# Optimization experiments

Hardware: AMD Instinct MI355X
Metric: run time of the kernel (lower is better)

## Reference

```python
import jax, jax.numpy as jnp
import numpy as np

N = 262144   # nodes
E = 1048576  # edges (avg degree 4)
DIN = 64     # input node features
H = 128      # hidden channels
DE = 32      # edge feature dim
EPS = 1e-5


def setup_inputs() -> dict:
    key = jax.random.key(0)
    ks = jax.random.split(key, 12)
    s = 0.05
    return {
        "x": jax.random.normal(ks[0], (N, DIN), jnp.float32),
        "edge_attr": jax.random.normal(ks[1], (E, DE), jnp.float32),
        "W_enter": jax.random.normal(ks[2], (H, DIN), jnp.float32) * s,
        "b_enter": jnp.zeros((H,), jnp.float32),
        "W1": jax.random.normal(ks[3], (H, H + DE), jnp.float32) * s,
        "att_l": jax.random.normal(ks[4], (H,), jnp.float32) * s,
        "att_r": jax.random.normal(ks[5], (H,), jnp.float32) * s,
        "W2": jax.random.normal(ks[6], (H, H), jnp.float32) * s,
        "b_conv": jnp.zeros((H,), jnp.float32),
        "W_ih": jax.random.normal(ks[7], (3 * H, H), jnp.float32) * s,
        "W_hh": jax.random.normal(ks[8], (3 * H, H), jnp.float32) * s,
        "b_ih": jnp.zeros((3 * H,), jnp.float32),
        "b_hh": jnp.zeros((3 * H,), jnp.float32),
        "edge_index": jax.random.randint(ks[9], (2, E), 0, N, jnp.int32),
    }


def _segment_softmax(logits, seg, num_segments):
    m = jax.ops.segment_max(logits, seg, num_segments=num_segments)
    e = jnp.exp(logits - m[seg])
    d = jax.ops.segment_sum(e, seg, num_segments=num_segments)
    return e / d[seg]


def reference(x, edge_attr, W_enter, b_enter, W1, att_l, att_r, W2, b_conv,
              W_ih, W_hh, b_ih, b_hh, edge_index):
    n = x.shape[0]
    src, dst = edge_index[0], edge_index[1]  # x_j = x[src], aggregate to dst

    # lin_enter + leaky_relu
    x = jax.nn.leaky_relu(x @ W_enter.T + b_enter)

    # Edge2dConv message: leaky_relu(lin1([x_j, edge_attr]))
    m = jax.nn.leaky_relu(jnp.concatenate([x[src], edge_attr], axis=-1) @ W1.T)  # [E,H]
    alpha = jax.nn.leaky_relu(m @ att_l + x[dst] @ att_r)  # [E]
    alpha = _segment_softmax(alpha, dst, n)
    msg = (m @ W2.T) * alpha[:, None]
    out = jax.ops.segment_sum(msg, dst, num_segments=n) + b_conv

    # elu, then GRUCell(h_in=out_elu, hidden=x)
    h = jax.nn.elu(out)
    gi = h @ W_ih.T + b_ih
    gh = x @ W_hh.T + b_hh
    ir, iz, inn = jnp.split(gi, 3, axis=-1)
    hr, hz, hn = jnp.split(gh, 3, axis=-1)
    r = jax.nn.sigmoid(ir + hr)
    z = jax.nn.sigmoid(iz + hz)
    ncand = jnp.tanh(inn + r * hn)
    x = jax.nn.relu((1.0 - z) * ncand + z * x)

    # layer_norm (no affine)
    mu = jnp.mean(x, axis=-1, keepdims=True)
    var = jnp.mean(jnp.square(x - mu), axis=-1, keepdims=True)
    return (x - mu) / jnp.sqrt(var + EPS)
```

## Files before the change

### kernel.cpp

```cpp
#include <hip/hip_runtime.h>
#include <stdint.h>

#define HD  128
#define DIN 64
#define DE  32

typedef unsigned int u32; typedef unsigned short u16; typedef unsigned char u8;
typedef short s16x8 __attribute__((ext_vector_type(8)));
typedef float f32x4 __attribute__((ext_vector_type(4)));
typedef float f32x2 __attribute__((ext_vector_type(2)));

#define MFMA16(a,b,c) __builtin_amdgcn_mfma_f32_16x16x32_bf16((a),(b),(c),0,0,0)

__device__ __forceinline__ float lrelu(float x){ return x > 0.f ? x : 0.01f*x; }
__device__ __forceinline__ float sigmoidf_(float x){ return 1.f/(1.f + __expf(-x)); }
__device__ __forceinline__ float tanhf_(float x){
    float t = fminf(fmaxf(x, -15.f), 15.f);
    float e = __expf(2.f*t);
    return (e - 1.f)/(e + 1.f);
}
__device__ __forceinline__ float eluf_(float x){ return x > 0.f ? x : expm1f(x); }

__device__ __forceinline__ u16 f32_to_bf16(float x){
    u32 u = __float_as_uint(x);
    u += 0x7FFFu + ((u >> 16) & 1u);
    return (u16)(u >> 16);
}
__device__ __forceinline__ float bf16lo(u32 u){ return __uint_as_float((u & 0xFFFFu) << 16); }
__device__ __forceinline__ float bf16hi(u32 u){ return __uint_as_float(u & 0xFFFF0000u); }
__device__ __forceinline__ float bf16f(u16 h){ return __uint_as_float(((u32)h) << 16); }
__device__ __forceinline__ u32 pk2(float a, float b){
    return (u32)f32_to_bf16(a) | ((u32)f32_to_bf16(b) << 16);
}
__device__ __forceinline__ u8 hw_f8(float v){
    return (u8)__builtin_amdgcn_cvt_pk_fp8_f32(v, v, 0, false);
}
__device__ __forceinline__ f32x2 hw_f8_dec2(u32 u){
    return __builtin_amdgcn_cvt_pk_f32_fp8((int)u, false);
}
__device__ __forceinline__ f32x2 hw_f8_dec2_hi(u32 u){
    return __builtin_amdgcn_cvt_pk_f32_fp8((int)u, true);
}

__device__ __forceinline__ float wave_max(float v){
    #pragma unroll
    for (int o = 32; o > 0; o >>= 1) v = fmaxf(v, __shfl_xor(v, o, 64));
    return v;
}
__device__ __forceinline__ float wave_sum(float v){
    #pragma unroll
    for (int o = 32; o > 0; o >>= 1) v += __shfl_xor(v, o, 64);
    return v;
}
__device__ __forceinline__ float dot8_bf16(uint4 v, const float* __restrict__ al){
    float d = 0.f;
    d = fmaf(bf16lo(v.x), al[0], d); d = fmaf(bf16hi(v.x), al[1], d);
    d = fmaf(bf16lo(v.y), al[2], d); d = fmaf(bf16hi(v.y), al[3], d);
    d = fmaf(bf16lo(v.z), al[4], d); d = fmaf(bf16hi(v.z), al[5], d);
    d = fmaf(bf16lo(v.w), al[6], d); d = fmaf(bf16hi(v.w), al[7], d);
    return d;
}

__global__ void k_prep(const float* __restrict__ W1, const float* __restrict__ W2,
                       const float* __restrict__ Went,
                       const float* __restrict__ Wih, const float* __restrict__ Whh,
                       u16* __restrict__ W1b, u16* __restrict__ W2b,
                       u16* __restrict__ Wentb, u16* __restrict__ Bg)
{
    int i = blockIdx.x*256 + threadIdx.x;
    if (i < 20480){ W1b[i] = f32_to_bf16(W1[i]); return; }
    i -= 20480;
    if (i < 16384){ W2b[i] = f32_to_bf16(W2[i]); return; }
    i -= 16384;
    if (i < 8192){ Wentb[i] = f32_to_bf16(Went[i]); return; }
    i -= 8192;
    if (i < 131072){
        int col = i >> 8, k = i & 255;
        int g = col >> 7, j = col & 127;
        float v;
        if      (g == 0) v = (k < 128) ? Wih[j*128 + k]        : Whh[j*128 + k - 128];
        else if (g == 1) v = (k < 128) ? Wih[(128+j)*128 + k]  : Whh[(128+j)*128 + k - 128];
        else if (g == 2) v = (k < 128) ? Wih[(256+j)*128 + k]  : 0.f;
        else             v = (k < 128) ? 0.f                   : Whh[(256+j)*128 + k - 128];
        Bg[i] = f32_to_bf16(v);
    }
}

__global__ void k_zero2(int* __restrict__ a, int* __restrict__ b, int n){
    int i = blockIdx.x*256 + threadIdx.x;
    if (i < n){ a[i] = 0; b[i] = 0; }
}

__global__ __launch_bounds__(256, 2) void k_enter_mfma(
    const float* __restrict__ x, const u16* __restrict__ Wb, const float* __restrict__ be,
    const float* __restrict__ att_r, u16* __restrict__ Ag, float* __restrict__ r_out, int N)
{
    __shared__ __align__(16) u8 sA[64*144];
    __shared__ __align__(16) u8 sO[64*272];
    int t = threadIdx.x, w = t >> 6, lane = t & 63, l15 = lane & 15, l4 = lane >> 4;
    int tile = blockIdx.x;

    s16x8 bfr[2][2];
    #pragma unroll
    for (int kf = 0; kf < 2; ++kf)
        #pragma unroll
        for (int cf = 0; cf < 2; ++cf)
            bfr[kf][cf] = *(const s16x8*)(Wb + (size_t)(w*32 + cf*16 + l15)*64 + kf*32 + l4*8);

    int el = t >> 2, q = t & 3;
    size_t n = (size_t)tile*64 + el;
    {
        const float4* xs = (const float4*)(x + n*64 + q*16);
        float4 f0 = xs[0], f1 = xs[1], f2 = xs[2], f3 = xs[3];
        uint4 o0, o1;
        o0.x = pk2(f0.x,f0.y); o0.y = pk2(f0.z,f0.w); o0.z = pk2(f1.x,f1.y); o0.w = pk2(f1.z,f1.w);
        o1.x = pk2(f2.x,f2.y); o1.y = pk2(f2.z,f2.w); o1.z = pk2(f3.x,f3.y); o1.w = pk2(f3.z,f3.w);
        *(uint4*)(sA + el*144 + q*32)      = o0;
        *(uint4*)(sA + el*144 + q*32 + 16) = o1;
    }
    __syncthreads();

    f32x4 acc[4][2];
    #pragma unroll
    for (int rf = 0; rf < 4; ++rf){ acc[rf][0] = (f32x4)0.f; acc[rf][1] = (f32x4)0.f; }
    #pragma unroll
    for (int kf = 0; kf < 2; ++kf){
        s16x8 a[4];
        #pragma unroll
        for (int rf = 0; rf < 4; ++rf)
            a[rf] = *(const s16x8*)(sA + (rf*16 + l15)*144 + kf*64 + l4*16);
        #pragma unroll
        for (int rf = 0; rf < 4; ++rf){
            acc[rf][0] = MFMA16(a[rf], bfr[kf][0], acc[rf][0]);
            acc[rf][1] = MFMA16(a[rf], bfr[kf][1], acc[rf][1]);
        }
    }
    float b0 = be[w*32 + l15], b1 = be[w*32 + 16 + l15];
    #pragma unroll
    for (int rf = 0; rf < 4; ++rf)
        #pragma unroll
        for (int r = 0; r < 4; ++r){
            int row = rf*16 + l4*4 + r;
            *(u16*)(sO + row*272 + (w*32 + l15)*2)      = f32_to_bf16(lrelu(acc[rf][0][r] + b0));
            *(u16*)(sO + row*272 + (w*32 + 16 + l15)*2) = f32_to_bf16(lrelu(acc[rf][1][r] + b1));
        }
    __syncthreads();

    float dot = 0.f;
    #pragma unroll
    for (int i = 0; i < 4; ++i){
        uint4 v = *(const uint4*)(sO + el*272 + q*64 + 16*i);
        ((uint4*)Ag)[n*32 + 16 + q*4 + i] = v;
        dot += dot8_bf16(v, att_r + q*32 + 8*i);
    }
    dot += __shfl_xor(dot, 1); dot += __shfl_xor(dot, 2);
    if (q == 0) r_out[n] = dot;
}

__global__ void k_hist(const int* __restrict__ dst, int* __restrict__ deg, int E){
    int e = blockIdx.x*256 + threadIdx.x;
    if (e < E) atomicAdd(&deg[dst[e]], 1);
}
__global__ __launch_bounds__(256) void k_scan_a(
    const int* __restrict__ deg, int* __restrict__ rs, int* __restrict__ btot, int N)
{
    __shared__ int sd[256];
    int b = blockIdx.x, t = threadIdx.x;
    int base = b*1024 + t*4;
    int d0 = deg[base], d1 = deg[base+1], d2 = deg[base+2], d3 = deg[base+3];
    int s = d0 + d1 + d2 + d3;
    sd[t] = s; __syncthreads();
    for (int o = 1; o < 256; o <<= 1){
        int v = (t >= o) ? sd[t-o] : 0;
        __syncthreads();
        sd[t] += v;
        __syncthreads();
    }
    int ex = sd[t] - s;
    rs[base]   = ex;
    rs[base+1] = ex + d0;
    rs[base+2] = ex + d0 + d1;
    rs[base+3] = ex + d0 + d1 + d2;
    if (t == 0) btot[b] = sd[255];
}
__global__ __launch_bounds__(256) void k_scan_b(const int* __restrict__ btot, int* __restrict__ bbase){
    __shared__ int sd[256];
    int t = threadIdx.x;
    int s = btot[t];
    sd[t] = s; __syncthreads();
    for (int o = 1; o < 256; o <<= 1){
        int v = (t >= o) ? sd[t-o] : 0;
        __syncthreads();
        sd[t] += v;
        __syncthreads();
    }
    bbase[t] = sd[t] - s;
}
__global__ void k_scan_c(int* __restrict__ rs, const int* __restrict__ bbase, int N, int E){
    int i = blockIdx.x*256 + threadIdx.x;
    if (i < N) rs[i] += bbase[i >> 10];
    if (i == 0) rs[N] = E;
}
__global__ void k_scatter(const int* __restrict__ dst, const int* __restrict__ rs,
                          int* __restrict__ cnt, int* __restrict__ epos, int E){
    int e = blockIdx.x*256 + threadIdx.x;
    if (e >= E) return;
    int d = dst[e];
    int pos = rs[d] + atomicAdd(&cnt[d], 1);
    epos[e] = pos;
}

__global__ __launch_bounds__(512, 4) void k_edge_mfma(
    const u16* __restrict__ Ag, const float* __restrict__ ea,
    const u16* __restrict__ W1b, const float* __restrict__ att_l,
    const float* __restrict__ r_dst, const int* __restrict__ src, const int* __restrict__ dst,
    const int* __restrict__ epos,
    u8* __restrict__ m, float* __restrict__ alpha, int ntiles, int E)
{
    __shared__ __align__(16) u8 sA[64*336];
    __shared__ __align__(16) u8 sM[64*144];
    int t = threadIdx.x, w = t >> 6, lane = t & 63, l15 = lane & 15, l4 = lane >> 4;

    s16x8 bfr[5];
    #pragma unroll
    for (int kf = 0; kf < 5; ++kf)
        bfr[kf] = *(const s16x8*)(W1b + (size_t)(w*16 + l15)*160 + kf*32 + l4*8);

    int el = t >> 3, q = t & 7;
    int stride = gridDim.x;
    int tile = blockIdx.x;

    uint4 cx0, cx1;
    u32 ce0, ce1;
    int   pe = 0;
    float rdv = 0.f;
    {
        int e = tile*64 + el;
        if (tile < ntiles && e < E){
            int sn = src[e];
            const uint4* xs = (const uint4*)Ag + (size_t)sn*32 + 16 + q*2;
            cx0 = xs[0]; cx1 = xs[1];
            float4 f = *(const float4*)(ea + (size_t)e*32 + q*4);
            ce0 = pk2(f.x, f.y); ce1 = pk2(f.z, f.w);
            pe  = epos[e];
            rdv = r_dst[dst[e]];
        }
    }

    int   ptile = -1;
    int   pe_prev = 0;
    float rdv_prev = 0.f;

    for (; tile < ntiles; tile += stride){
        int e = tile*64 + el;
        if (e < E){
            uint4* d = (uint4*)(sA + el*336 + q*32);
            d[0] = cx0; d[1] = cx1;
            *(u32*)(sA + el*336 + 256 + q*8)     = ce0;
            *(u32*)(sA + el*336 + 256 + q*8 + 4) = ce1;
        }
        int pe_cur = pe; float rdv_cur = rdv;

        int nt = tile + stride;
        if (nt < ntiles){
            int e2 = nt*64 + el;
            if (e2 < E){
                int sn = src[e2];
                const uint4* xs = (const uint4*)Ag + (size_t)sn*32 + 16 + q*2;
                cx0 = xs[0]; cx1 = xs[1];
                float4 f = *(const float4*)(ea + (size_t)e2*32 + q*4);
                ce0 = pk2(f.x, f.y); ce1 = pk2(f.z, f.w);
                pe  = epos[e2];
                rdv = r_dst[dst[e2]];
            }
        }

        if (ptile >= 0){
            int ep = ptile*64 + el;
            if (ep < E){
                uint4 v = *(const uint4*)(sM + el*144 + q*16);
                ((uint4*)m)[(size_t)pe_prev*8 + q] = v;
                u32 ws[4] = {v.x, v.y, v.z, v.w};
                float dotv = 0.f;
                #pragma unroll
                for (int i = 0; i < 4; ++i){
                    f32x2 fa = hw_f8_dec2(ws[i]);
                    f32x2 fb = hw_f8_dec2_hi(ws[i]);
                    const float* al = att_l + q*16 + i*4;
                    dotv = fmaf(fa.x, al[0], dotv); dotv = fmaf(fa.y, al[1], dotv);
                    dotv = fmaf(fb.x, al[2], dotv); dotv = fmaf(fb.y, al[3], dotv);
                }
                dotv += __shfl_xor(dotv, 1); dotv += __shfl_xor(dotv, 2); dotv += __shfl_xor(dotv, 4);
                if (q == 0) alpha[pe_prev] = lrelu(dotv + rdv_prev);
            }
        }
        __syncthreads();

        f32x4 acc[4];
        #pragma unroll
        for (int rf = 0; rf < 4; ++rf) acc[rf] = (f32x4)0.f;
        #pragma unroll
        for (int kf = 0; kf < 5; ++kf){
            s16x8 a[4];
            #pragma unroll
            for (int rf = 0; rf < 4; ++rf)
                a[rf] = *(const s16x8*)(sA + (rf*16 + l15)*336 + kf*64 + l4*16);
            #pragma unroll
            for (int rf = 0; rf < 4; ++rf)
                acc[rf] = MFMA16(a[rf], bfr[kf], acc[rf]);
        }

        int col = w*16 + l15;
        #pragma unroll
        for (int rf = 0; rf < 4; ++rf)
            #pragma unroll
            for (int r = 0; r < 4; ++r){
                int row = rf*16 + l4*4 + r;
                sM[row*144 + col] = hw_f8(lrelu(acc[rf][r]));
            }
        __syncthreads();

        ptile = tile; pe_prev = pe_cur; rdv_prev = rdv_cur;
    }

    if (ptile >= 0){
        int ep = ptile*64 + el;
        if (ep < E){
            uint4 v = *(const uint4*)(sM + el*144 + q*16);
            ((uint4*)m)[(size_t)pe_prev*8 + q] = v;
            u32 ws[4] = {v.x, v.y, v.z, v.w};
            float dotv = 0.f;
            #pragma unroll
            for (int i = 0; i < 4; ++i){
                f32x2 fa = hw_f8_dec2(ws[i]);
                f32x2 fb = hw_f8_dec2_hi(ws[i]);
                const float* al = att_l + q*16 + i*4;
                dotv = fmaf(fa.x, al[0], dotv); dotv = fmaf(fa.y, al[1], dotv);
                dotv = fmaf(fb.x, al[2], dotv); dotv = fmaf(fb.y, al[3], dotv);
            }
            dotv += __shfl_xor(dotv, 1); dotv += __shfl_xor(dotv, 2); dotv += __shfl_xor(dotv, 4);
            if (q == 0) alpha[pe_prev] = lrelu(dotv + rdv_prev);
        }
    }
}

__global__ __launch_bounds__(256) void k_agg(
    const int* __restrict__ rs,
    const float* __restrict__ alpha, const u8* __restrict__ m,
    u16* __restrict__ a_out, int N)
{
    int wid  = (blockIdx.x*256 + threadIdx.x) >> 6;
    int lane = threadIdx.x & 63;
    if (wid >= N) return;
    int s = rs[wid], t = rs[wid+1];
    int deg = t - s;
    float ax = 0.f, ay = 0.f;
    if (deg > 0 && deg <= 64){
        float av = -1e38f;
        if (lane < deg) av = alpha[s + lane];
        float mx = wave_max(av);
        float ev = (lane < deg) ? __expf(av - mx) : 0.f;
        float ssum = wave_sum(ev);
        float wreg = ev / ssum;
        int k = 0;
        for (; k + 2 <= deg; k += 2){
            float w0 = __shfl(wreg, k);
            float w1 = __shfl(wreg, k + 1);
            u32 u0 = *(const u16*)(m + (size_t)(s + k)*HD + 2*lane);
            u32 u1 = *(const u16*)(m + (size_t)(s + k + 1)*HD + 2*lane);
            f32x2 f0 = hw_f8_dec2(u0);
            f32x2 f1 = hw_f8_dec2(u1);
            ax = fmaf(w0, f0.x, ax); ay = fmaf(w0, f0.y, ay);
            ax = fmaf(w1, f1.x, ax); ay = fmaf(w1, f1.y, ay);
        }
        if (k < deg){
            float w0 = __shfl(wreg, k);
            u32 u0 = *(const u16*)(m + (size_t)(s + k)*HD + 2*lane);
            f32x2 f0 = hw_f8_dec2(u0);
            ax = fmaf(w0, f0.x, ax); ay = fmaf(w0, f0.y, ay);
        }
    } else if (deg > 64){
        float mx = -1e38f;
        for (int k = lane; k < deg; k += 64) mx = fmaxf(mx, alpha[s + k]);
        mx = wave_max(mx);
        float ssum = 0.f;
        for (int k = lane; k < deg; k += 64) ssum += __expf(alpha[s + k] - mx);
        ssum = wave_sum(ssum);
        float inv = 1.f / ssum;
        for (int k = 0; k < deg; ++k){
            float wgt = __expf(alpha[s + k] - mx) * inv;
            u32 u0 = *(const u16*)(m + (size_t)(s + k)*HD + 2*lane);
            f32x2 f0 = hw_f8_dec2(u0);
            ax = fmaf(wgt, f0.x, ax);
            ay = fmaf(wgt, f0.y, ay);
        }
    }
    *(u32*)(a_out + (size_t)wid*HD + 2*lane) = pk2(ax, ay);
}

__global__ __launch_bounds__(256, 2) void k_conv2_mfma(
    const u16* __restrict__ a, const u16* __restrict__ W2b, const float* __restrict__ bc,
    u16* __restrict__ Ag, int N)
{
    __shared__ __align__(16) u8 sA[64*272];
    __shared__ __align__(16) u8 sO[64*272];
    int t = threadIdx.x, w = t >> 6, lane = t & 63, l15 = lane & 15, l4 = lane >> 4;
    int tile = blockIdx.x;

    s16x8 bfr[4][2];
    #pragma unroll
    for (int kf = 0; kf < 4; ++kf)
        #pragma unroll
        for (int cf = 0; cf < 2; ++cf)
            bfr[kf][cf] = *(const s16x8*)(W2b + (size_t)(w*32 + cf*16 + l15)*128 + kf*32 + l4*8);

    int el = t >> 2, q = t & 3;
    size_t n = (size_t)tile*64 + el;
    {
        const uint4* as = (const uint4*)(a + n*HD) + q*4;
        uint4 v0 = as[0], v1 = as[1], v2 = as[2], v3 = as[3];
        uint4* d = (uint4*)(sA + el*272 + q*64);
        d[0] = v0; d[1] = v1; d[2] = v2; d[3] = v3;
    }
    __syncthreads();

    f32x4 acc[4][2];
    #pragma unroll
    for (int rf = 0; rf < 4; ++rf){ acc[rf][0] = (f32x4)0.f; acc[rf][1] = (f32x4)0.f; }
    #pragma unroll
    for (int kf = 0; kf < 4; ++kf){
        s16x8 av[4];
        #pragma unroll
        for (int rf = 0; rf < 4; ++rf)
            av[rf] = *(const s16x8*)(sA + (rf*16 + l15)*272 + kf*64 + l4*16);
        #pragma unroll
        for (int rf = 0; rf < 4; ++rf){
            acc[rf][0] = MFMA16(av[rf], bfr[kf][0], acc[rf][0]);
            acc[rf][1] = MFMA16(av[rf], bfr[kf][1], acc[rf][1]);
        }
    }
    float b0 = bc[w*32 + l15], b1 = bc[w*32 + 16 + l15];
    #pragma unroll
    for (int rf = 0; rf < 4; ++rf)
        #pragma unroll
        for (int r = 0; r < 4; ++r){
            int row = rf*16 + l4*4 + r;
            *(u16*)(sO + row*272 + (w*32 + l15)*2)      = f32_to_bf16(eluf_(acc[rf][0][r] + b0));
            *(u16*)(sO + row*272 + (w*32 + 16 + l15)*2) = f32_to_bf16(eluf_(acc[rf][1][r] + b1));
        }
    __syncthreads();
    #pragma unroll
    for (int i = 0; i < 4; ++i){
        uint4 v = *(const uint4*)(sO + el*272 + q*64 + 16*i);
        ((uint4*)Ag)[n*32 + q*4 + i] = v;
    }
}

__global__ __launch_bounds__(512, 3) void k_gru_mfma(
    const u16* __restrict__ Ag, const u16* __restrict__ Bg,
    const float* __restrict__ bih, const float* __restrict__ bhh,
    float* __restrict__ out, int N, int ntiles)
{
    __shared__ __align__(16) u8 sA[32*528];
    __shared__ __align__(16) float sOut[32*132];
    int t = threadIdx.x, w = t >> 6, lane = t & 63, l15 = lane & 15, l4 = lane >> 4;

    s16x8 bfr0[8], bfr1[8], bfr2[4], bfr3[4];
    {
        int jc = w*16 + l15;
        #pragma unroll
        for (int kf = 0; kf < 8; ++kf){
            bfr0[kf] = *(const s16x8*)(Bg + (size_t)(jc)*256       + kf*32 + l4*8);
            bfr1[kf] = *(const s16x8*)(Bg + (size_t)(128 + jc)*256 + kf*32 + l4*8);
        }
        #pragma unroll
        for (int kf = 0; kf < 4; ++kf){
            bfr2[kf] = *(const s16x8*)(Bg + (size_t)(256 + jc)*256 + kf*32 + l4*8);
            bfr3[kf] = *(const s16x8*)(Bg + (size_t)(384 + jc)*256 + (kf+4)*32 + l4*8);
        }
    }
    int j = w*16 + l15;
    float rb = bih[j] + bhh[j];
    float zb = bih[128 + j] + bhh[128 + j];
    float ib = bih[256 + j];
    float hb = bhh[256 + j];

    int el = t >> 4, part = t & 15;
    int stride = gridDim.x;
    int tile = blockIdx.x;
    uint4 pv0, pv1;
    if (tile < ntiles){
        const uint4* gsrc = (const uint4*)Ag + ((size_t)tile*32 + el)*32 + part*2;
        pv0 = gsrc[0]; pv1 = gsrc[1];
    }

    for (; tile < ntiles; tile += stride){
        {
            uint4* d = (uint4*)(sA + el*528 + part*32);
            d[0] = pv0; d[1] = pv1;
        }
        __syncthreads();

        int nt = tile + stride;
        if (nt < ntiles){
            const uint4* gsrc = (const uint4*)Ag + ((size_t)nt*32 + el)*32 + part*2;
            pv0 = gsrc[0]; pv1 = gsrc[1];
        }

        f32x4 acc[2][4];
        #pragma unroll
        for (int rf = 0; rf < 2; ++rf)
            #pragma unroll
            for (int g = 0; g < 4; ++g) acc[rf][g] = (f32x4)0.f;
        #pragma unroll
        for (int kf = 0; kf < 8; ++kf){
            s16x8 a0 = *(const s16x8*)(sA + l15*528 + kf*64 + l4*16);
            s16x8 a1 = *(const s16x8*)(sA + (16 + l15)*528 + kf*64 + l4*16);
            acc[0][0] = MFMA16(a0, bfr0[kf], acc[0][0]);
            acc[1][0] = MFMA16(a1, bfr0[kf], acc[1][0]);
            acc[0][1] = MFMA16(a0, bfr1[kf], acc[0][1]);
            acc[1][1] = MFMA16(a1, bfr1[kf], acc[1][1]);
            if (kf < 4){
                acc[0][2] = MFMA16(a0, bfr2[kf], acc[0][2]);
                acc[1][2] = MFMA16(a1, bfr2[kf], acc[1][2]);
            } else {
                acc[0][3] = MFMA16(a0, bfr3[kf-4], acc[0][3]);
                acc[1][3] = MFMA16(a1, bfr3[kf-4], acc[1][3]);
            }
        }
        #pragma unroll
        for (int rf = 0; rf < 2; ++rf)
            #pragma unroll
            for (int r = 0; r < 4; ++r){
                int rl = rf*16 + l4*4 + r;
                float rr = sigmoidf_(acc[rf][0][r] + rb);
                float zz = sigmoidf_(acc[rf][1][r] + zb);
                float iv = acc[rf][2][r] + ib;
                float hv = acc[rf][3][r] + hb;
                float nc = tanhf_(iv + rr*hv);
                float xej = bf16f(*(const u16*)(sA + rl*528 + 256 + 2*j));
                float v = (1.f - zz)*nc + zz*xej;
                v = fmaxf(v, 0.f);
                sOut[rl*132 + j] = v;
            }
        __syncthreads();
        {
            int row = t >> 4, sub = t & 15;
            const float* rp = sOut + row*132 + sub*8;
            float v0 = rp[0], v1 = rp[1], v2 = rp[2], v3 = rp[3];
            float v4 = rp[4], v5 = rp[5], v6 = rp[6], v7 = rp[7];
            float s1 = v0+v1+v2+v3+v4+v5+v6+v7;
            float s2 = v0*v0+v1*v1+v2*v2+v3*v3+v4*v4+v5*v5+v6*v6+v7*v7;
            #pragma unroll
            for (int o = 1; o < 16; o <<= 1){ s1 += __shfl_xor(s1, o); s2 += __shfl_xor(s2, o); }
            float mu  = s1 * (1.f/128.f);
            float var = s2 * (1.f/128.f) - mu*mu;
            var = fmaxf(var, 0.f);
            float rsd = rsqrtf(var + 1e-5f);
            float* op = out + ((size_t)tile*32 + row)*128 + sub*8;
            float4 o0, o1;
            o0.x = (v0-mu)*rsd; o0.y = (v1-mu)*rsd; o0.z = (v2-mu)*rsd; o0.w = (v3-mu)*rsd;
            o1.x = (v4-mu)*rsd; o1.y = (v5-mu)*rsd; o1.z = (v6-mu)*rsd; o1.w = (v7-mu)*rsd;
            ((float4*)op)[0] = o0; ((float4*)op)[1] = o1;
        }
        __syncthreads();
    }
}

extern "C" void kernel_launch(void* const* d_in, const int* in_sizes, int n_in,
                              void* d_out, int out_size, void* d_ws, size_t ws_size,
                              hipStream_t stream)
{
    const float* x       = (const float*)d_in[0];
    const float* ea      = (const float*)d_in[1];
    const float* W_enter = (const float*)d_in[2];
    const float* b_enter = (const float*)d_in[3];
    const float* W1      = (const float*)d_in[4];
    const float* att_l   = (const float*)d_in[5];
    const float* att_r   = (const float*)d_in[6];
    const float* W2      = (const float*)d_in[7];
    const float* b_conv  = (const float*)d_in[8];
    const float* W_ih    = (const float*)d_in[9];
    const float* W_hh    = (const float*)d_in[10];
    const float* b_ih    = (const float*)d_in[11];
    const float* b_hh    = (const float*)d_in[12];
    const int*   eidx    = (const int*)d_in[13];

    int N = in_sizes[0] / DIN;
    int E = in_sizes[13] / 2;
    const int* src = eidx;
    const int* dst = eidx + E;
    float* out = (float*)d_out;

    size_t off = 0;
    char* base = (char*)d_ws;
    auto alloc = [&](size_t bytes) -> char* {
        char* p = base + off;
        off = (off + bytes + 255) & ~(size_t)255;
        return p;
    };
    u16*   Ag    = (u16*)  alloc((size_t)N*256*2);
    float* r_dst = (float*)alloc((size_t)N*4);
    float* alpha = (float*)alloc((size_t)E*4);
    int*   deg   = (int*)  alloc((size_t)N*4);
    int*   rs    = (int*)  alloc((size_t)(N+1)*4);
    int*   cnt   = (int*)  alloc((size_t)N*4);
    int*   epos  = (int*)  alloc((size_t)E*4);
    int*   btot  = (int*)  alloc(1024);
    int*   bbase = (int*)  alloc(1024);
    u16*   W1b   = (u16*)  alloc(20480*2);
    u16*   W2b   = (u16*)  alloc(16384*2);
    u16*   Wentb = (u16*)  alloc(8192*2);
    u16*   Bg    = (u16*)  alloc(131072*2);
    u8*    mbuf  = (u8*)   alloc((size_t)E*HD);

    u16* a_agg = (u16*)out;

    int ntiles_n64 = N/64, ntiles_e = (E + 63)/64, ntiles_g = N/32;

    k_prep   <<<(176128+255)/256, 256, 0, stream>>>(W1, W2, W_enter, W_ih, W_hh, W1b, W2b, Wentb, Bg);
    k_zero2  <<<(N+255)/256, 256, 0, stream>>>(deg, cnt, N);
    k_enter_mfma<<<ntiles_n64, 256, 0, stream>>>(x, Wentb, b_enter, att_r, Ag, r_dst, N);
    k_hist   <<<(E+255)/256, 256, 0, stream>>>(dst, deg, E);
    k_scan_a <<<N/1024, 256, 0, stream>>>(deg, rs, btot, N);
    k_scan_b <<<1, 256, 0, stream>>>(btot, bbase);
    k_scan_c <<<(N+255)/256, 256, 0, stream>>>(rs, bbase, N, E);
    k_scatter<<<(E+255)/256, 256, 0, stream>>>(dst, rs, cnt, epos, E);
    k_edge_mfma<<<1024, 512, 0, stream>>>(Ag, ea, W1b, att_l, r_dst, src, dst, epos,
                                          mbuf, alpha, ntiles_e, E);
    k_agg    <<<(N+3)/4, 256, 0, stream>>>(rs, alpha, mbuf, a_agg, N);
    k_conv2_mfma<<<ntiles_n64, 256, 0, stream>>>(a_agg, W2b, b_conv, Ag, N);
    k_gru_mfma  <<<2048, 512, 0, stream>>>(Ag, Bg, b_ih, b_hh, out, N, ntiles_g);
}
```

Measured before the change: 597.2 us.

## Run GRU GEMM in fp8 and split node buffer into bf16 features and fp8 GRU input

```diff
diff --git a/kernel.cpp b/kernel.cpp
--- a/kernel.cpp
+++ b/kernel.cpp
@@ -6,11 +6,13 @@
 #define DE  32
 
 typedef unsigned int u32; typedef unsigned short u16; typedef unsigned char u8;
+typedef long i64_;
 typedef short s16x8 __attribute__((ext_vector_type(8)));
 typedef float f32x4 __attribute__((ext_vector_type(4)));
 typedef float f32x2 __attribute__((ext_vector_type(2)));
 
-#define MFMA16(a,b,c) __builtin_amdgcn_mfma_f32_16x16x32_bf16((a),(b),(c),0,0,0)
+#define MFMA16(a,b,c)  __builtin_amdgcn_mfma_f32_16x16x32_bf16((a),(b),(c),0,0,0)
+#define MFMAF8(a,b,c)  __builtin_amdgcn_mfma_f32_16x16x32_fp8_fp8((a),(b),(c),0,0,0)
 
 __device__ __forceinline__ float lrelu(float x){ return x > 0.f ? x : 0.01f*x; }
 __device__ __forceinline__ float sigmoidf_(float x){ return 1.f/(1.f + __expf(-x)); }
@@ -34,6 +36,11 @@
 }
 __device__ __forceinline__ u8 hw_f8(float v){
     return (u8)__builtin_amdgcn_cvt_pk_fp8_f32(v, v, 0, false);
+}
+__device__ __forceinline__ u32 hw_f8x4(float a, float b, float c, float d){
+    u32 r = (u32)__builtin_amdgcn_cvt_pk_fp8_f32(a, b, 0, false);
+    r = (u32)__builtin_amdgcn_cvt_pk_fp8_f32(c, d, (int)r, true);
+    return r;
 }
 __device__ __forceinline__ f32x2 hw_f8_dec2(u32 u){
     return __builtin_amdgcn_cvt_pk_f32_fp8((int)u, false);
@@ -65,7 +72,7 @@
                        const float* __restrict__ Went,
                        const float* __restrict__ Wih, const float* __restrict__ Whh,
                        u16* __restrict__ W1b, u16* __restrict__ W2b,
-                       u16* __restrict__ Wentb, u16* __restrict__ Bg)
+                       u16* __restrict__ Wentb, u8* __restrict__ Bgf8)
 {
     int i = blockIdx.x*256 + threadIdx.x;
     if (i < 20480){ W1b[i] = f32_to_bf16(W1[i]); return; }
@@ -82,7 +89,7 @@
         else if (g == 1) v = (k < 128) ? Wih[(128+j)*128 + k]  : Whh[(128+j)*128 + k - 128];
         else if (g == 2) v = (k < 128) ? Wih[(256+j)*128 + k]  : 0.f;
         else             v = (k < 128) ? 0.f                   : Whh[(256+j)*128 + k - 128];
-        Bg[i] = f32_to_bf16(v);
+        Bgf8[i] = hw_f8(v);
     }
 }
 
@@ -93,7 +100,8 @@
 
 __global__ __launch_bounds__(256, 2) void k_enter_mfma(
     const float* __restrict__ x, const u16* __restrict__ Wb, const float* __restrict__ be,
-    const float* __restrict__ att_r, u16* __restrict__ Ag, float* __restrict__ r_out, int N)
+    const float* __restrict__ att_r, u16* __restrict__ xeb, u8* __restrict__ Agru,
+    float* __restrict__ r_out, int N)
 {
     __shared__ __align__(16) u8 sA[64*144];
     __shared__ __align__(16) u8 sO[64*272];
@@ -150,8 +158,16 @@
     #pragma unroll
     for (int i = 0; i < 4; ++i){
         uint4 v = *(const uint4*)(sO + el*272 + q*64 + 16*i);
-        ((uint4*)Ag)[n*32 + 16 + q*4 + i] = v;
-        dot += dot8_bf16(v, att_r + q*32 + 8*i);
+        ((uint4*)xeb)[n*16 + q*4 + i] = v;
+        float f0 = bf16lo(v.x), f1 = bf16hi(v.x), f2 = bf16lo(v.y), f3 = bf16hi(v.y);
+        float f4 = bf16lo(v.z), f5 = bf16hi(v.z), f6 = bf16lo(v.w), f7 = bf16hi(v.w);
+        const float* al = att_r + q*32 + 8*i;
+        dot = fmaf(f0, al[0], dot); dot = fmaf(f1, al[1], dot);
+        dot = fmaf(f2, al[2], dot); dot = fmaf(f3, al[3], dot);
+        dot = fmaf(f4, al[4], dot); dot = fmaf(f5, al[5], dot);
+        dot = fmaf(f6, al[6], dot); dot = fmaf(f7, al[7], dot);
+        uint2 p; p.x = hw_f8x4(f0, f1, f2, f3); p.y = hw_f8x4(f4, f5, f6, f7);
+        *(uint2*)(Agru + n*256 + 128 + q*32 + i*8) = p;
     }
     dot += __shfl_xor(dot, 1); dot += __shfl_xor(dot, 2);
     if (q == 0) r_out[n] = dot;
@@ -211,7 +227,7 @@
 }
 
 __global__ __launch_bounds__(512, 4) void k_edge_mfma(
-    const u16* __restrict__ Ag, const float* __restrict__ ea,
+    const u16* __restrict__ xeb, const float* __restrict__ ea,
     const u16* __restrict__ W1b, const float* __restrict__ att_l,
     const float* __restrict__ r_dst, const int* __restrict__ src, const int* __restrict__ dst,
     const int* __restrict__ epos,
@@ -238,7 +254,7 @@
         int e = tile*64 + el;
         if (tile < ntiles && e < E){
             int sn = src[e];
-            const uint4* xs = (const uint4*)Ag + (size_t)sn*32 + 16 + q*2;
+            const uint4* xs = (const uint4*)xeb + (size_t)sn*16 + q*2;
             cx0 = xs[0]; cx1 = xs[1];
             float4 f = *(const float4*)(ea + (size_t)e*32 + q*4);
             ce0 = pk2(f.x, f.y); ce1 = pk2(f.z, f.w);
@@ -266,7 +282,7 @@
             int e2 = nt*64 + el;
             if (e2 < E){
                 int sn = src[e2];
-                const uint4* xs = (const uint4*)Ag + (size_t)sn*32 + 16 + q*2;
+                const uint4* xs = (const uint4*)xeb + (size_t)sn*16 + q*2;
                 cx0 = xs[0]; cx1 = xs[1];
                 float4 f = *(const float4*)(ea + (size_t)e2*32 + q*4);
                 ce0 = pk2(f.x, f.y); ce1 = pk2(f.z, f.w);
@@ -400,7 +416,7 @@
 
 __global__ __launch_bounds__(256, 2) void k_conv2_mfma(
     const u16* __restrict__ a, const u16* __restrict__ W2b, const float* __restrict__ bc,
-    u16* __restrict__ Ag, int N)
+    u8* __restrict__ Agru, int N)
 {
     __shared__ __align__(16) u8 sA[64*272];
     __shared__ __align__(16) u8 sO[64*272];
@@ -452,31 +468,35 @@
     #pragma unroll
     for (int i = 0; i < 4; ++i){
         uint4 v = *(const uint4*)(sO + el*272 + q*64 + 16*i);
-        ((uint4*)Ag)[n*32 + q*4 + i] = v;
-    }
-}
-
-__global__ __launch_bounds__(512, 3) void k_gru_mfma(
-    const u16* __restrict__ Ag, const u16* __restrict__ Bg,
+        float f0 = bf16lo(v.x), f1 = bf16hi(v.x), f2 = bf16lo(v.y), f3 = bf16hi(v.y);
+        float f4 = bf16lo(v.z), f5 = bf16hi(v.z), f6 = bf16lo(v.w), f7 = bf16hi(v.w);
+        uint2 p; p.x = hw_f8x4(f0, f1, f2, f3); p.y = hw_f8x4(f4, f5, f6, f7);
+        *(uint2*)(Agru + n*256 + q*32 + i*8) = p;
+    }
+}
+
+__global__ __launch_bounds__(512, 4) void k_gru_mfma(
+    const u8* __restrict__ Agru, const u16* __restrict__ xeb, const u8* __restrict__ Bgf8,
     const float* __restrict__ bih, const float* __restrict__ bhh,
     float* __restrict__ out, int N, int ntiles)
 {
-    __shared__ __align__(16) u8 sA[32*528];
+    __shared__ __align__(16) u8 sA[32*272];
+    __shared__ __align__(16) u8 sX[32*272];
     __shared__ __align__(16) float sOut[32*132];
     int t = threadIdx.x, w = t >> 6, lane = t & 63, l15 = lane & 15, l4 = lane >> 4;
 
-    s16x8 bfr0[8], bfr1[8], bfr2[4], bfr3[4];
+    i64_ bfr0[8], bfr1[8], bfr2[4], bfr3[4];
     {
         int jc = w*16 + l15;
         #pragma unroll
         for (int kf = 0; kf < 8; ++kf){
-            bfr0[kf] = *(const s16x8*)(Bg + (size_t)(jc)*256       + kf*32 + l4*8);
-            bfr1[kf] = *(const s16x8*)(Bg + (size_t)(128 + jc)*256 + kf*32 + l4*8);
+            bfr0[kf] = *(const i64_*)(Bgf8 + (size_t)(jc)*256       + kf*32 + l4*8);
+            bfr1[kf] = *(const i64_*)(Bgf8 + (size_t)(128 + jc)*256 + kf*32 + l4*8);
         }
         #pragma unroll
         for (int kf = 0; kf < 4; ++kf){
-            bfr2[kf] = *(const s16x8*)(Bg + (size_t)(256 + jc)*256 + kf*32 + l4*8);
-            bfr3[kf] = *(const s16x8*)(Bg + (size_t)(384 + jc)*256 + (kf+4)*32 + l4*8);
+            bfr2[kf] = *(const i64_*)(Bgf8 + (size_t)(256 + jc)*256 + kf*32 + l4*8);
+            bfr3[kf] = *(const i64_*)(Bgf8 + (size_t)(384 + jc)*256 + (kf+4)*32 + l4*8);
         }
     }
     int j = w*16 + l15;
@@ -488,23 +508,21 @@
     int el = t >> 4, part = t & 15;
     int stride = gridDim.x;
     int tile = blockIdx.x;
-    uint4 pv0, pv1;
+    uint4 pa, px;
     if (tile < ntiles){
-        const uint4* gsrc = (const uint4*)Ag + ((size_t)tile*32 + el)*32 + part*2;
-        pv0 = gsrc[0]; pv1 = gsrc[1];
+        pa = *((const uint4*)Agru + ((size_t)tile*32 + el)*16 + part);
+        px = *((const uint4*)xeb  + ((size_t)tile*32 + el)*16 + part);
     }
 
     for (; tile < ntiles; tile += stride){
-        {
-            uint4* d = (uint4*)(sA + el*528 + part*32);
-            d[0] = pv0; d[1] = pv1;
-        }
+        *(uint4*)(sA + el*272 + part*16) = pa;
+        *(uint4*)(sX + el*272 + part*16) = px;
         __syncthreads();
 
         int nt = tile + stride;
         if (nt < ntiles){
-            const uint4* gsrc = (const uint4*)Ag + ((size_t)nt*32 + el)*32 + part*2;
-            pv0 = gsrc[0]; pv1 = gsrc[1];
+            pa = *((const uint4*)Agru + ((size_t)nt*32 + el)*16 + part);
+            px = *((const uint4*)xeb  + ((size_t)nt*32 + el)*16 + part);
         }
 
         f32x4 acc[2][4];
@@ -514,18 +532,18 @@
             for (int g = 0; g < 4; ++g) acc[rf][g] = (f32x4)0.f;
         #pragma unroll
         for (int kf = 0; kf < 8; ++kf){
-            s16x8 a0 = *(const s16x8*)(sA + l15*528 + kf*64 + l4*16);
-            s16x8 a1 = *(const s16x8*)(sA + (16 + l15)*528 + kf*64 + l4*16);
-            acc[0][0] = MFMA16(a0, bfr0[kf], acc[0][0]);
-            acc[1][0] = MFMA16(a1, bfr0[kf], acc[1][0]);
-            acc[0][1] = MFMA16(a0, bfr1[kf], acc[0][1]);
-            acc[1][1] = MFMA16(a1, bfr1[kf], acc[1][1]);
+            i64_ a0 = *(const i64_*)(sA + l15*272 + kf*32 + l4*8);
+            i64_ a1 = *(const i64_*)(sA + (16 + l15)*272 + kf*32 + l4*8);
+            acc[0][0] = MFMAF8(a0, bfr0[kf], acc[0][0]);
+            acc[1][0] = MFMAF8(a1, bfr0[kf], acc[1][0]);
+            acc[0][1] = MFMAF8(a0, bfr1[kf], acc[0][1]);
+            acc[1][1] = MFMAF8(a1, bfr1[kf], acc[1][1]);
             if (kf < 4){
-                acc[0][2] = MFMA16(a0, bfr2[kf], acc[0][2]);
-                acc[1][2] = MFMA16(a1, bfr2[kf], acc[1][2]);
+                acc[0][2] = MFMAF8(a0, bfr2[kf], acc[0][2]);
+                acc[1][2] = MFMAF8(a1, bfr2[kf], acc[1][2]);
             } else {
-                acc[0][3] = MFMA16(a0, bfr3[kf-4], acc[0][3]);
-                acc[1][3] = MFMA16(a1, bfr3[kf-4], acc[1][3]);
+                acc[0][3] = MFMAF8(a0, bfr3[kf-4], acc[0][3]);
+                acc[1][3] = MFMAF8(a1, bfr3[kf-4], acc[1][3]);
             }
         }
         #pragma unroll
@@ -538,7 +556,7 @@
                 float iv = acc[rf][2][r] + ib;
                 float hv = acc[rf][3][r] + hb;
                 float nc = tanhf_(iv + rr*hv);
-                float xej = bf16f(*(const u16*)(sA + rl*528 + 256 + 2*j));
+                float xej = bf16f(*(const u16*)(sX + rl*272 + 2*j));
                 float v = (1.f - zz)*nc + zz*xej;
                 v = fmaxf(v, 0.f);
                 sOut[rl*132 + j] = v;
@@ -599,7 +617,8 @@
         off = (off + bytes + 255) & ~(size_t)255;
         return p;
     };
-    u16*   Ag    = (u16*)  alloc((size_t)N*256*2);
+    u16*   xeb   = (u16*)  alloc((size_t)N*HD*2);
+    u8*    Agru  = (u8*)   alloc((size_t)N*256);
     float* r_dst = (float*)alloc((size_t)N*4);
     float* alpha = (float*)alloc((size_t)E*4);
     int*   deg   = (int*)  alloc((size_t)N*4);
@@ -611,24 +630,24 @@
     u16*   W1b   = (u16*)  alloc(20480*2);
     u16*   W2b   = (u16*)  alloc(16384*2);
     u16*   Wentb = (u16*)  alloc(8192*2);
-    u16*   Bg    = (u16*)  alloc(131072*2);
+    u8*    Bgf8  = (u8*)   alloc(131072);
     u8*    mbuf  = (u8*)   alloc((size_t)E*HD);
 
     u16* a_agg = (u16*)out;
 
     int ntiles_n64 = N/64, ntiles_e = (E + 63)/64, ntiles_g = N/32;
 
-    k_prep   <<<(176128+255)/256, 256, 0, stream>>>(W1, W2, W_enter, W_ih, W_hh, W1b, W2b, Wentb, Bg);
+    k_prep   <<<(176128+255)/256, 256, 0, stream>>>(W1, W2, W_enter, W_ih, W_hh, W1b, W2b, Wentb, Bgf8);
     k_zero2  <<<(N+255)/256, 256, 0, stream>>>(deg, cnt, N);
-    k_enter_mfma<<<ntiles_n64, 256, 0, stream>>>(x, Wentb, b_enter, att_r, Ag, r_dst, N);
+    k_enter_mfma<<<ntiles_n64, 256, 0, stream>>>(x, Wentb, b_enter, att_r, xeb, Agru, r_dst, N);
     k_hist   <<<(E+255)/256, 256, 0, stream>>>(dst, deg, E);
     k_scan_a <<<N/1024, 256, 0, stream>>>(deg, rs, btot, N);
     k_scan_b <<<1, 256, 0, stream>>>(btot, bbase);
     k_scan_c <<<(N+255)/256, 256, 0, stream>>>(rs, bbase, N, E);
     k_scatter<<<(E+255)/256, 256, 0, stream>>>(dst, rs, cnt, epos, E);
-    k_edge_mfma<<<1024, 512, 0, stream>>>(Ag, ea, W1b, att_l, r_dst, src, dst, epos,
+    k_edge_mfma<<<1024, 512, 0, stream>>>(xeb, ea, W1b, att_l, r_dst, src, dst, epos,
                                           mbuf, alpha, ntiles_e, E);
     k_agg    <<<(N+3)/4, 256, 0, stream>>>(rs, alpha, mbuf, a_agg, N);
-    k_conv2_mfma<<<ntiles_n64, 256, 0, stream>>>(a_agg, W2b, b_conv, Ag, N);
-    k_gru_mfma  <<<2048, 512, 0, stream>>>(Ag, Bg, b_ih, b_hh, out, N, ntiles_g);
-}
+    k_conv2_mfma<<<ntiles_n64, 256, 0, stream>>>(a_agg, W2b, b_conv, Agru, N);
+    k_gru_mfma  <<<2048, 512, 0, stream>>>(Agru, xeb, Bgf8, b_ih, b_hh, out, N, ntiles_g);
+}
```

After: 548.9 us. 8.1% less time.
